# Kernel optimization log

Hardware: AMD Instinct MI355X
Metric: run time of the kernel (lower is better)

Reference implementation:

```python
import jax, jax.numpy as jnp
import numpy as np

TEMPERATURE = 0.02


def setup_inputs() -> dict:
    key = jax.random.key(0)
    kq, kp = jax.random.split(key)
    query_embeddings = jax.random.normal(kq, (32, 32, 128), dtype=jnp.float32)      # [b, s, h]
    positive_embeddings = jax.random.normal(kp, (512, 128, 128), dtype=jnp.float32)  # [c, d, h]
    return {"query_embeddings": query_embeddings, "positive_embeddings": positive_embeddings}


def reference(query_embeddings, positive_embeddings):
    # Late interaction: all query tokens vs all doc tokens across the (in-)batch.
    # [b, c, s, d]
    late = jnp.einsum('bsh,cdh->bcsd', query_embeddings, positive_embeddings)
    # MaxSim: max over doc tokens, sum over query tokens -> [b, c]
    scores = late.max(axis=-1).sum(axis=-1) / TEMPERATURE
    # CrossEntropyLoss(reduction='mean') with labels = zeros(b)
    loss = jnp.mean(jax.nn.logsumexp(scores, axis=-1) - scores[:, 0])
    return loss
```

## Files before the change

### kernel.cpp

```cpp
#include <hip/hip_runtime.h>

#define BQ 32
#define H  128
#define C  512
#define D  128

typedef _Float16 half8v __attribute__((ext_vector_type(8)));
typedef float floatx4 __attribute__((ext_vector_type(4)));

__global__ __launch_bounds__(256) void qprep_kernel(const float* __restrict__ q,
                                                    _Float16* __restrict__ qs,
                                                    float* __restrict__ out) {
  int t = blockIdx.x * 256 + threadIdx.x;
  if (t == 0) out[0] = 0.0f;
  int lane = t & 63;
  int sh   = (t >> 6) & 1;
  int kb   = (t >> 7) & 3;
  int b    = t >> 9;
  int s    = sh * 16 + (lane & 15);
  int h    = kb * 32 + (lane >> 4) * 8;
  const float* src = q + ((b * 32 + s) * H + h);
  float4 v0 = *(const float4*)src;
  float4 v1 = *(const float4*)(src + 4);
  half8v o = { (_Float16)v0.x, (_Float16)v0.y, (_Float16)v0.z, (_Float16)v0.w,
               (_Float16)v1.x, (_Float16)v1.y, (_Float16)v1.z, (_Float16)v1.w };
  *(half8v*)(qs + (size_t)t * 8) = o;
}

__global__ __launch_bounds__(256, 2) void scores_kernel(const float* __restrict__ pos,
                                                        const _Float16* __restrict__ qs,
                                                        float* __restrict__ scores) {
  const int c    = blockIdx.x;
  const int tid  = threadIdx.x;
  const int w    = tid >> 6;
  const int lane = tid & 63;
  const int dq   = w & 1;
  const int sh   = w >> 1;
  const int quad = lane >> 4;
  const int nrow = lane & 15;

  __shared__ float pmm[BQ][4][16];

  const half8v* qf = (const half8v*)qs;
  const float*  pc = pos + (size_t)c * (D * H);

  half8v  pa[4][4];
  half8v  qb[3][4];
  floatx4 acc[2][4];
  floatx4 zc = {0.f, 0.f, 0.f, 0.f};

#pragma unroll
  for (int kb = 0; kb < 4; ++kb)
#pragma unroll
    for (int mt = 0; mt < 4; ++mt) {
      const float* src = pc + ((dq * 64 + mt * 16 + nrow) * H + kb * 32 + quad * 8);
      float4 v0 = *(const float4*)src;
      float4 v1 = *(const float4*)(src + 4);
      half8v f = { (_Float16)v0.x, (_Float16)v0.y, (_Float16)v0.z, (_Float16)v0.w,
                   (_Float16)v1.x, (_Float16)v1.y, (_Float16)v1.z, (_Float16)v1.w };
      pa[mt][kb] = f;
    }

#pragma unroll
  for (int kb = 0; kb < 4; ++kb) qb[0][kb] = qf[(kb * 2 + sh) * 64 + lane];
#pragma unroll
  for (int kb = 0; kb < 4; ++kb) qb[1][kb] = qf[((4 + kb) * 2 + sh) * 64 + lane];

  auto reduce_store = [&](int b, floatx4 (&a)[4]) {
    float m0 = fmaxf(fmaxf(a[0][0], a[0][1]), fmaxf(a[0][2], a[0][3]));
    float m1 = fmaxf(fmaxf(a[1][0], a[1][1]), fmaxf(a[1][2], a[1][3]));
    float m2 = fmaxf(fmaxf(a[2][0], a[2][1]), fmaxf(a[2][2], a[2][3]));
    float m3 = fmaxf(fmaxf(a[3][0], a[3][1]), fmaxf(a[3][2], a[3][3]));
    float m  = fmaxf(fmaxf(m0, m1), fmaxf(m2, m3));
    m = fmaxf(m, __shfl_xor(m, 16));
    m = fmaxf(m, __shfl_xor(m, 32));
    if (lane < 16) pmm[b][w][lane] = m;
  };

#pragma unroll
  for (int b = 0; b < BQ; ++b) {
    const int cur = b & 1;
    if (b + 2 < BQ) {
      half8v* dst = qb[(b + 2) % 3];
#pragma unroll
      for (int kb = 0; kb < 4; ++kb) dst[kb] = qf[(((b + 2) * 4 + kb) * 2 + sh) * 64 + lane];
    }
    const half8v* qc = qb[b % 3];
#pragma unroll
    for (int mt = 0; mt < 4; ++mt)
      acc[cur][mt] = __builtin_amdgcn_mfma_f32_16x16x32_f16(pa[mt][0], qc[0], zc, 0, 0, 0);
#pragma unroll
    for (int kb = 1; kb < 4; ++kb)
#pragma unroll
      for (int mt = 0; mt < 4; ++mt)
        acc[cur][mt] = __builtin_amdgcn_mfma_f32_16x16x32_f16(pa[mt][kb], qc[kb], acc[cur][mt], 0, 0, 0);
    if (b > 0) reduce_store(b - 1, acc[cur ^ 1]);
  }
  reduce_store(BQ - 1, acc[1]);

  __syncthreads();

  {
    int b  = tid >> 3;
    int t8 = tid & 7;
    float v = 0.f;
#pragma unroll
    for (int j = 0; j < 4; ++j) {
      int s  = t8 * 4 + j;
      int h2 = s >> 4, sl = s & 15;
      v += fmaxf(pmm[b][2 * h2][sl], pmm[b][2 * h2 + 1][sl]);
    }
    v += __shfl_xor(v, 1);
    v += __shfl_xor(v, 2);
    v += __shfl_xor(v, 4);
    if (t8 == 0) scores[b * C + c] = v * 50.0f;
  }
}

__global__ __launch_bounds__(256) void loss_kernel(const float* __restrict__ scores,
                                                   float* __restrict__ out) {
  __shared__ float red[8];
  const int b = blockIdx.x, tid = threadIdx.x, w = tid >> 6, lane = tid & 63;
  const float* row = scores + b * C;
  float x0 = row[tid], x1 = row[tid + 256];
  float mx = fmaxf(x0, x1);
#pragma unroll
  for (int off = 1; off < 64; off <<= 1) mx = fmaxf(mx, __shfl_xor(mx, off));
  if (lane == 0) red[w] = mx;
  __syncthreads();
  float bmax = fmaxf(fmaxf(red[0], red[1]), fmaxf(red[2], red[3]));
  float e = __expf(x0 - bmax) + __expf(x1 - bmax);
#pragma unroll
  for (int off = 1; off < 64; off <<= 1) e += __shfl_xor(e, off);
  if (lane == 0) red[4 + w] = e;
  __syncthreads();
  if (tid == 0) {
    float s = red[4] + red[5] + red[6] + red[7];
    atomicAdd(out, (bmax + __logf(s) - row[0]) * (1.0f / 32.0f));
  }
}

extern "C" void kernel_launch(void* const* d_in, const int* in_sizes, int n_in,
                              void* d_out, int out_size, void* d_ws, size_t ws_size,
                              hipStream_t stream) {
  const float* q = (const float*)d_in[0];
  const float* p = (const float*)d_in[1];
  float* scores  = (float*)d_ws;
  _Float16* qs   = (_Float16*)((char*)d_ws + 65536);

  qprep_kernel<<<64, 256, 0, stream>>>(q, qs, (float*)d_out);
  scores_kernel<<<C, 256, 0, stream>>>(p, qs, scores);
  loss_kernel<<<32, 256, 0, stream>>>(scores, (float*)d_out);
}
```

Before: 93.81 us.

## Stage query fragments into shared LDS ring via async global-to-LDS loads

Each block now handles two documents with 512 threads and shares the query fragments through a 4-slot LDS ring filled by global_load_lds, replacing the per-wave register prefetch of queries from global memory. This cuts redundant global/L2 traffic for the query tensor, since eight waves share one staged copy. In exchange, a block-wide barrier and vmcnt wait are added every batch iteration, which may stall waves and serialise MFMA work. The grid is halved to 256 blocks, which fewer than the CU count may leave part of the GPU idle.

```diff
diff --git a/kernel.cpp b/kernel.cpp
--- a/kernel.cpp
+++ b/kernel.cpp
@@ -7,6 +7,13 @@
 
 typedef _Float16 half8v __attribute__((ext_vector_type(8)));
 typedef float floatx4 __attribute__((ext_vector_type(4)));
+
+typedef const __attribute__((address_space(1))) unsigned int* gas_u32;
+typedef __attribute__((address_space(3))) unsigned int* las_u32;
+
+__device__ __forceinline__ void stage16(const void* g, void* l) {
+  __builtin_amdgcn_global_load_lds((gas_u32)g, (las_u32)l, 16, 0, 0);
+}
 
 __global__ __launch_bounds__(256) void qprep_kernel(const float* __restrict__ q,
                                                     _Float16* __restrict__ qs,
@@ -27,28 +34,30 @@
   *(half8v*)(qs + (size_t)t * 8) = o;
 }
 
-__global__ __launch_bounds__(256, 2) void scores_kernel(const float* __restrict__ pos,
+__global__ __launch_bounds__(512, 2) void scores_kernel(const float* __restrict__ pos,
                                                         const _Float16* __restrict__ qs,
                                                         float* __restrict__ scores) {
-  const int c    = blockIdx.x;
+  const int bx   = blockIdx.x;
   const int tid  = threadIdx.x;
   const int w    = tid >> 6;
   const int lane = tid & 63;
-  const int dq   = w & 1;
-  const int sh   = w >> 1;
+  const int cs   = w >> 2;
+  const int w4   = w & 3;
+  const int dq   = w4 & 1;
+  const int sh   = w4 >> 1;
   const int quad = lane >> 4;
   const int nrow = lane & 15;
 
-  __shared__ float pmm[BQ][4][16];
+  __shared__ __align__(16) _Float16 qring[4][8][512];
+  __shared__ float pmm[2][BQ][4][16];
 
-  const half8v* qf = (const half8v*)qs;
-  const float*  pc = pos + (size_t)c * (D * H);
+  const char* qbytes = (const char*)qs;
 
-  half8v  pa[4][4];
-  half8v  qb[3][4];
-  floatx4 acc[2][4];
-  floatx4 zc = {0.f, 0.f, 0.f, 0.f};
+  stage16(qbytes + ((0 * 8 + w) << 10) + lane * 16, &qring[0][w][0]);
+  stage16(qbytes + ((1 * 8 + w) << 10) + lane * 16, &qring[1][w][0]);
 
+  const float* pc = pos + (size_t)(2 * bx + cs) * (D * H);
+  half8v pa[4][4];
 #pragma unroll
   for (int kb = 0; kb < 4; ++kb)
 #pragma unroll
@@ -61,10 +70,8 @@
       pa[mt][kb] = f;
     }
 
-#pragma unroll
-  for (int kb = 0; kb < 4; ++kb) qb[0][kb] = qf[(kb * 2 + sh) * 64 + lane];
-#pragma unroll
-  for (int kb = 0; kb < 4; ++kb) qb[1][kb] = qf[((4 + kb) * 2 + sh) * 64 + lane];
+  floatx4 acc[2][4];
+  floatx4 zc = {0.f, 0.f, 0.f, 0.f};
 
   auto reduce_store = [&](int b, floatx4 (&a)[4]) {
     float m0 = fmaxf(fmaxf(a[0][0], a[0][1]), fmaxf(a[0][2], a[0][3]));
@@ -74,26 +81,39 @@
     float m  = fmaxf(fmaxf(m0, m1), fmaxf(m2, m3));
     m = fmaxf(m, __shfl_xor(m, 16));
     m = fmaxf(m, __shfl_xor(m, 32));
-    if (lane < 16) pmm[b][w][lane] = m;
+    if (lane < 16) pmm[cs][b][w4][lane] = m;
   };
 
 #pragma unroll
   for (int b = 0; b < BQ; ++b) {
     const int cur = b & 1;
-    if (b + 2 < BQ) {
-      half8v* dst = qb[(b + 2) % 3];
-#pragma unroll
-      for (int kb = 0; kb < 4; ++kb) dst[kb] = qf[(((b + 2) * 4 + kb) * 2 + sh) * 64 + lane];
+    {
+      const int srcs = (b + 2 < BQ) ? (b + 2) : (BQ - 1);
+      const int slot = (b + 2) & 3;
+      stage16(qbytes + ((srcs * 8 + w) << 10) + lane * 16, &qring[slot][w][0]);
     }
-    const half8v* qc = qb[b % 3];
+    __builtin_amdgcn_sched_barrier(0);
+    asm volatile("s_waitcnt vmcnt(2)" ::: "memory");
+    __builtin_amdgcn_s_barrier();
+    __builtin_amdgcn_sched_barrier(0);
+
+    const int rs = b & 3;
+    const half8v q0 = *(const half8v*)&qring[rs][0 + sh][(size_t)lane * 8];
+    const half8v q1 = *(const half8v*)&qring[rs][2 + sh][(size_t)lane * 8];
+    const half8v q2 = *(const half8v*)&qring[rs][4 + sh][(size_t)lane * 8];
+    const half8v q3 = *(const half8v*)&qring[rs][6 + sh][(size_t)lane * 8];
 #pragma unroll
     for (int mt = 0; mt < 4; ++mt)
-      acc[cur][mt] = __builtin_amdgcn_mfma_f32_16x16x32_f16(pa[mt][0], qc[0], zc, 0, 0, 0);
+      acc[cur][mt] = __builtin_amdgcn_mfma_f32_16x16x32_f16(pa[mt][0], q0, zc, 0, 0, 0);
 #pragma unroll
-    for (int kb = 1; kb < 4; ++kb)
+    for (int mt = 0; mt < 4; ++mt)
+      acc[cur][mt] = __builtin_amdgcn_mfma_f32_16x16x32_f16(pa[mt][1], q1, acc[cur][mt], 0, 0, 0);
 #pragma unroll
-      for (int mt = 0; mt < 4; ++mt)
-        acc[cur][mt] = __builtin_amdgcn_mfma_f32_16x16x32_f16(pa[mt][kb], qc[kb], acc[cur][mt], 0, 0, 0);
+    for (int mt = 0; mt < 4; ++mt)
+      acc[cur][mt] = __builtin_amdgcn_mfma_f32_16x16x32_f16(pa[mt][2], q2, acc[cur][mt], 0, 0, 0);
+#pragma unroll
+    for (int mt = 0; mt < 4; ++mt)
+      acc[cur][mt] = __builtin_amdgcn_mfma_f32_16x16x32_f16(pa[mt][3], q3, acc[cur][mt], 0, 0, 0);
     if (b > 0) reduce_store(b - 1, acc[cur ^ 1]);
   }
   reduce_store(BQ - 1, acc[1]);
@@ -101,19 +121,21 @@
   __syncthreads();
 
   {
-    int b  = tid >> 3;
-    int t8 = tid & 7;
+    int cs2 = tid >> 8;
+    int r   = tid & 255;
+    int b   = r >> 3;
+    int t8  = r & 7;
     float v = 0.f;
 #pragma unroll
     for (int j = 0; j < 4; ++j) {
       int s  = t8 * 4 + j;
       int h2 = s >> 4, sl = s & 15;
-      v += fmaxf(pmm[b][2 * h2][sl], pmm[b][2 * h2 + 1][sl]);
+      v += fmaxf(pmm[cs2][b][2 * h2][sl], pmm[cs2][b][2 * h2 + 1][sl]);
     }
     v += __shfl_xor(v, 1);
     v += __shfl_xor(v, 2);
     v += __shfl_xor(v, 4);
-    if (t8 == 0) scores[b * C + c] = v * 50.0f;
+    if (t8 == 0) scores[b * C + (2 * bx + cs2)] = v * 50.0f;
   }
 }
 
@@ -149,6 +171,6 @@
   _Float16* qs   = (_Float16*)((char*)d_ws + 65536);
 
   qprep_kernel<<<64, 256, 0, stream>>>(q, qs, (float*)d_out);
-  scores_kernel<<<C, 256, 0, stream>>>(p, qs, scores);
+  scores_kernel<<<256, 512, 0, stream>>>(p, qs, scores);
   loss_kernel<<<32, 256, 0, stream>>>(scores, (float*)d_out);
 }
```

After: 97.99 us. +4.5%, slower.

## Fuse query fp16 conversion into scores kernel and use single-block loss

Applied to the files above, without the earlier changes.

Drops the separate query-prep kernel. Each scores block now loads fp32 query rows directly and converts them to fp16 in registers, double-buffering the raw float4 loads. The loss kernel becomes a single 512-thread block that handles all 32 rows and writes the result directly, replacing the zero-init plus atomicAdd. This removes one kernel launch and the atomic, at the cost of doubled query load bytes and redundant conversions in every one of the 512 blocks, plus extra register pressure from fp32 staging.

```diff
diff --git a/kernel.cpp b/kernel.cpp
--- a/kernel.cpp
+++ b/kernel.cpp
@@ -8,27 +8,8 @@
 typedef _Float16 half8v __attribute__((ext_vector_type(8)));
 typedef float floatx4 __attribute__((ext_vector_type(4)));
 
-__global__ __launch_bounds__(256) void qprep_kernel(const float* __restrict__ q,
-                                                    _Float16* __restrict__ qs,
-                                                    float* __restrict__ out) {
-  int t = blockIdx.x * 256 + threadIdx.x;
-  if (t == 0) out[0] = 0.0f;
-  int lane = t & 63;
-  int sh   = (t >> 6) & 1;
-  int kb   = (t >> 7) & 3;
-  int b    = t >> 9;
-  int s    = sh * 16 + (lane & 15);
-  int h    = kb * 32 + (lane >> 4) * 8;
-  const float* src = q + ((b * 32 + s) * H + h);
-  float4 v0 = *(const float4*)src;
-  float4 v1 = *(const float4*)(src + 4);
-  half8v o = { (_Float16)v0.x, (_Float16)v0.y, (_Float16)v0.z, (_Float16)v0.w,
-               (_Float16)v1.x, (_Float16)v1.y, (_Float16)v1.z, (_Float16)v1.w };
-  *(half8v*)(qs + (size_t)t * 8) = o;
-}
-
 __global__ __launch_bounds__(256, 2) void scores_kernel(const float* __restrict__ pos,
-                                                        const _Float16* __restrict__ qs,
+                                                        const float* __restrict__ q,
                                                         float* __restrict__ scores) {
   const int c    = blockIdx.x;
   const int tid  = threadIdx.x;
@@ -41,14 +22,22 @@
 
   __shared__ float pmm[BQ][4][16];
 
-  const half8v* qf = (const half8v*)qs;
-  const float*  pc = pos + (size_t)c * (D * H);
+  const float* qsrc = q + ((sh * 16 + nrow) * H + quad * 8);
 
-  half8v  pa[4][4];
-  half8v  qb[3][4];
-  floatx4 acc[2][4];
-  floatx4 zc = {0.f, 0.f, 0.f, 0.f};
+  float4 qsl[2][4][2];
+#pragma unroll
+  for (int kb = 0; kb < 4; ++kb) {
+    qsl[0][kb][0] = *(const float4*)(qsrc + 0 * (BQ * H) + kb * 32);
+    qsl[0][kb][1] = *(const float4*)(qsrc + 0 * (BQ * H) + kb * 32 + 4);
+  }
+#pragma unroll
+  for (int kb = 0; kb < 4; ++kb) {
+    qsl[1][kb][0] = *(const float4*)(qsrc + 1 * (BQ * H) + kb * 32);
+    qsl[1][kb][1] = *(const float4*)(qsrc + 1 * (BQ * H) + kb * 32 + 4);
+  }
 
+  const float* pc = pos + (size_t)c * (D * H);
+  half8v pa[4][4];
 #pragma unroll
   for (int kb = 0; kb < 4; ++kb)
 #pragma unroll
@@ -61,10 +50,8 @@
       pa[mt][kb] = f;
     }
 
-#pragma unroll
-  for (int kb = 0; kb < 4; ++kb) qb[0][kb] = qf[(kb * 2 + sh) * 64 + lane];
-#pragma unroll
-  for (int kb = 0; kb < 4; ++kb) qb[1][kb] = qf[((4 + kb) * 2 + sh) * 64 + lane];
+  floatx4 acc[2][4];
+  floatx4 zc = {0.f, 0.f, 0.f, 0.f};
 
   auto reduce_store = [&](int b, floatx4 (&a)[4]) {
     float m0 = fmaxf(fmaxf(a[0][0], a[0][1]), fmaxf(a[0][2], a[0][3]));
@@ -80,12 +67,24 @@
 #pragma unroll
   for (int b = 0; b < BQ; ++b) {
     const int cur = b & 1;
+    const int s   = b & 1;
+    half8v qc[4];
+#pragma unroll
+    for (int kb = 0; kb < 4; ++kb) {
+      float4 v0 = qsl[s][kb][0];
+      float4 v1 = qsl[s][kb][1];
+      half8v f = { (_Float16)v0.x, (_Float16)v0.y, (_Float16)v0.z, (_Float16)v0.w,
+                   (_Float16)v1.x, (_Float16)v1.y, (_Float16)v1.z, (_Float16)v1.w };
+      qc[kb] = f;
+    }
     if (b + 2 < BQ) {
-      half8v* dst = qb[(b + 2) % 3];
+      const float* nb = qsrc + (size_t)(b + 2) * (BQ * H);
 #pragma unroll
-      for (int kb = 0; kb < 4; ++kb) dst[kb] = qf[(((b + 2) * 4 + kb) * 2 + sh) * 64 + lane];
+      for (int kb = 0; kb < 4; ++kb) {
+        qsl[s][kb][0] = *(const float4*)(nb + kb * 32);
+        qsl[s][kb][1] = *(const float4*)(nb + kb * 32 + 4);
+      }
     }
-    const half8v* qc = qb[b % 3];
 #pragma unroll
     for (int mt = 0; mt < 4; ++mt)
       acc[cur][mt] = __builtin_amdgcn_mfma_f32_16x16x32_f16(pa[mt][0], qc[0], zc, 0, 0, 0);
@@ -117,26 +116,33 @@
   }
 }
 
-__global__ __launch_bounds__(256) void loss_kernel(const float* __restrict__ scores,
+__global__ __launch_bounds__(512) void loss_kernel(const float* __restrict__ scores,
                                                    float* __restrict__ out) {
   __shared__ float red[8];
-  const int b = blockIdx.x, tid = threadIdx.x, w = tid >> 6, lane = tid & 63;
-  const float* row = scores + b * C;
-  float x0 = row[tid], x1 = row[tid + 256];
-  float mx = fmaxf(x0, x1);
+  const int tid = threadIdx.x, w = tid >> 6, lane = tid & 63;
+  float part = 0.f;
 #pragma unroll
-  for (int off = 1; off < 64; off <<= 1) mx = fmaxf(mx, __shfl_xor(mx, off));
-  if (lane == 0) red[w] = mx;
-  __syncthreads();
-  float bmax = fmaxf(fmaxf(red[0], red[1]), fmaxf(red[2], red[3]));
-  float e = __expf(x0 - bmax) + __expf(x1 - bmax);
+  for (int i = 0; i < 4; ++i) {
+    const int b = w * 4 + i;
+    const float* row = scores + b * C;
+    const float4* r4 = (const float4*)row;
+    float4 v0 = r4[lane * 2];
+    float4 v1 = r4[lane * 2 + 1];
+    float mx = fmaxf(fmaxf(fmaxf(v0.x, v0.y), fmaxf(v0.z, v0.w)),
+                     fmaxf(fmaxf(v1.x, v1.y), fmaxf(v1.z, v1.w)));
 #pragma unroll
-  for (int off = 1; off < 64; off <<= 1) e += __shfl_xor(e, off);
-  if (lane == 0) red[4 + w] = e;
+    for (int off = 1; off < 64; off <<= 1) mx = fmaxf(mx, __shfl_xor(mx, off));
+    float e = __expf(v0.x - mx) + __expf(v0.y - mx) + __expf(v0.z - mx) + __expf(v0.w - mx)
+            + __expf(v1.x - mx) + __expf(v1.y - mx) + __expf(v1.z - mx) + __expf(v1.w - mx);
+#pragma unroll
+    for (int off = 1; off < 64; off <<= 1) e += __shfl_xor(e, off);
+    if (lane == 0) part += mx + __logf(e) - row[0];
+  }
+  if (lane == 0) red[w] = part;
   __syncthreads();
   if (tid == 0) {
-    float s = red[4] + red[5] + red[6] + red[7];
-    atomicAdd(out, (bmax + __logf(s) - row[0]) * (1.0f / 32.0f));
+    float s = red[0] + red[1] + red[2] + red[3] + red[4] + red[5] + red[6] + red[7];
+    out[0] = s * (1.0f / 32.0f);
   }
 }
 
@@ -146,9 +152,7 @@
   const float* q = (const float*)d_in[0];
   const float* p = (const float*)d_in[1];
   float* scores  = (float*)d_ws;
-  _Float16* qs   = (_Float16*)((char*)d_ws + 65536);
 
-  qprep_kernel<<<64, 256, 0, stream>>>(q, qs, (float*)d_out);
-  scores_kernel<<<C, 256, 0, stream>>>(p, qs, scores);
-  loss_kernel<<<32, 256, 0, stream>>>(scores, (float*)d_out);
+  scores_kernel<<<C, 256, 0, stream>>>(p, q, scores);
+  loss_kernel<<<1, 512, 0, stream>>>(scores, (float*)d_out);
 }
```

Measured after the change: 139.9 us. +49.2%, slower.
